# Kernel optimization log

Hardware: AMD Instinct MI355X
Metric: run time of the kernel (lower is better)

Reference implementation:

```python
import jax, jax.numpy as jnp
import numpy as np


def _degree_norms(src, dst, num_nodes, dtype):
    ones = jnp.ones(src.shape[0], dtype=dtype)
    out_deg = jax.ops.segment_sum(ones, src, num_segments=num_nodes)
    in_deg = jax.ops.segment_sum(ones, dst, num_segments=num_nodes)
    # DGL clamps degrees to min 1 (allow_zero_in_degree=True path)
    norm_src = jax.lax.rsqrt(jnp.maximum(out_deg, 1.0))  # D_out^{-1/2}
    norm_dst = jax.lax.rsqrt(jnp.maximum(in_deg, 1.0))   # D_in^{-1/2}
    return norm_src, norm_dst


def _graph_conv(x, W, b, src, dst, norm_src, norm_dst, num_nodes):
    # h = D_in^{-1/2} A D_out^{-1/2} x W + b  (DGL GraphConv, norm='both')
    h = x * norm_src[:, None]                                   # [N, d_in]
    agg = jax.ops.segment_sum(h[src], dst, num_segments=num_nodes)  # gather-scatter SpMM
    agg = agg * norm_dst[:, None]
    return agg @ W + b


def setup_inputs() -> dict:
    key = jax.random.key(0)
    k1, k2, k3, k4, k5 = jax.random.split(key, 5)
    N, E, D_IN, D_OUT = 100000, 1600000, 128, 64
    feature = jax.random.normal(k1, (N, D_IN), dtype=jnp.float32)
    src = jax.random.randint(k2, (E,), 0, N, dtype=jnp.int64)
    dst = jax.random.randint(k3, (E,), 0, N, dtype=jnp.int64)
    W1 = jax.random.normal(k4, (D_IN, D_IN), dtype=jnp.float32) / np.sqrt(D_IN)
    b1 = jnp.zeros((D_IN,), dtype=jnp.float32)
    W2 = jax.random.normal(k5, (D_IN, D_OUT), dtype=jnp.float32) / np.sqrt(D_IN)
    b2 = jnp.zeros((D_OUT,), dtype=jnp.float32)
    return {"feature": feature, "src": src, "dst": dst,
            "W1": W1, "b1": b1, "W2": W2, "b2": b2}


def reference(feature, src, dst, W1, b1, W2, b2):
    N = feature.shape[0]
    norm_src, norm_dst = _degree_norms(src, dst, N, feature.dtype)
    out = _graph_conv(feature, W1, b1, src, dst, norm_src, norm_dst, N)
    out = jax.nn.relu(out)
    # dropout is identity in eval mode (correctness baseline)
    out = _graph_conv(out, W2, b2, src, dst, norm_src, norm_dst, N)
    return out
```

## Files before the change

kernel.cpp:

```cpp
#include <hip/hip_runtime.h>

#define DIN 128
#define PB 512
typedef unsigned short u16;
typedef unsigned int u32;
typedef __attribute__((ext_vector_type(8))) short bf16x8;
typedef __attribute__((ext_vector_type(4))) float f32x4;

static __device__ __forceinline__ float bf2f(u32 lo16) {
    union { u32 u; float f; } c;
    c.u = lo16 << 16;
    return c.f;
}
static __device__ __forceinline__ float bf_lo(u32 v) {
    union { u32 u; float f; } c;
    c.u = v << 16;
    return c.f;
}
static __device__ __forceinline__ float bf_hi(u32 v) {
    union { u32 u; float f; } c;
    c.u = v & 0xffff0000u;
    return c.f;
}
static __device__ __forceinline__ u32 f2bf(float f) {
    union { float f; u32 u; } c;
    c.f = f;
    u32 u = c.u;
    u += 0x7fffu + ((u >> 16) & 1u);
    return u >> 16;
}

static __device__ __forceinline__ int wave_incl_scan(int x, int lane) {
#pragma unroll
    for (int off = 1; off < 64; off <<= 1) {
        int y = __shfl_up(x, off, 64);
        if (lane >= off) x += y;
    }
    return x;
}

__global__ __launch_bounds__(256) void hist_kernel(
    const int* __restrict__ src, const int* __restrict__ dst,
    u32* __restrict__ mat, int E, int NB, int M) {
    __shared__ u32 hd[512], hs[512];
    int t = threadIdx.x, b = blockIdx.x;
    for (int j = t; j < NB; j += 256) { hd[j] = 0; hs[j] = 0; }
    __syncthreads();
    int chunk = (E + PB - 1) / PB;
    int s = b * chunk, e = min(E, s + chunk);
    for (int i = s + t; i < e; i += 256) {
        atomicAdd(&hd[((u32)dst[i]) >> 8], 1u);
        atomicAdd(&hs[((u32)src[i]) >> 8], 1u);
    }
    __syncthreads();
    for (int j = t; j < NB; j += 256) {
        mat[(size_t)j * PB + b] = hd[j];
        mat[(size_t)M + (size_t)j * PB + b] = hs[j];
    }
}

__global__ void scan_block_kernel(const int* __restrict__ in, int* __restrict__ out,
                                  int* __restrict__ bsums, int n) {
    __shared__ int wsum[4];
    int i = blockIdx.x * 256 + threadIdx.x;
    int lane = threadIdx.x & 63, wid = threadIdx.x >> 6;
    int v = (i < n) ? in[i] : 0;
    int sc = wave_incl_scan(v, lane);
    if (lane == 63) wsum[wid] = sc;
    __syncthreads();
    int add = 0;
    for (int w = 0; w < wid; ++w) add += wsum[w];
    if (i < n) out[i] = sc - v + add;
    if (threadIdx.x == 255) bsums[blockIdx.x] = sc + add;
}

__global__ void scan_sums_kernel(int* __restrict__ bsums, int nb) {
    __shared__ int wsum[4];
    __shared__ int carry;
    int lane = threadIdx.x & 63, wid = threadIdx.x >> 6;
    if (threadIdx.x == 0) carry = 0;
    __syncthreads();
    for (int base = 0; base < nb; base += 256) {
        int i = base + threadIdx.x;
        int v = (i < nb) ? bsums[i] : 0;
        int sc = wave_incl_scan(v, lane);
        if (lane == 63) wsum[wid] = sc;
        __syncthreads();
        int add = carry;
        for (int w = 0; w < wid; ++w) add += wsum[w];
        if (i < nb) bsums[i] = sc - v + add;
        __syncthreads();
        if (threadIdx.x == 0) carry += wsum[0] + wsum[1] + wsum[2] + wsum[3];
        __syncthreads();
    }
}

__global__ void add_off2_kernel(int* __restrict__ out, const int* __restrict__ bsums, int n) {
    int i = blockIdx.x * 256 + threadIdx.x;
    if (i < n) out[i] += bsums[i >> 8];
}

__global__ __launch_bounds__(256) void part_kernel(
    const int* __restrict__ src, const int* __restrict__ dst,
    const int* __restrict__ off, u32* __restrict__ part, int E, int NB, int M) {
    __shared__ u32 cd[512], cs[512];
    int t = threadIdx.x, b = blockIdx.x;
    for (int j = t; j < NB; j += 256) {
        cd[j] = (u32)off[(size_t)j * PB + b];
        cs[j] = (u32)off[(size_t)M + (size_t)j * PB + b];
    }
    __syncthreads();
    int chunk = (E + PB - 1) / PB;
    int s = b * chunk, e = min(E, s + chunk);
    for (int i = s + t; i < e; i += 256) {
        u32 dv = (u32)dst[i], sv = (u32)src[i];
        u32 p = atomicAdd(&cd[dv >> 8], 1u);
        part[p] = ((dv & 255u) << 24) | sv;
        u32 q = atomicAdd(&cs[sv >> 8], 1u);
        part[q] = sv;
    }
}

__global__ __launch_bounds__(256) void build_kernel(
    const u32* __restrict__ part, const int* __restrict__ off,
    int* __restrict__ rowptr, float* __restrict__ nd, float* __restrict__ ns,
    int* __restrict__ csr_src, int N, int E, int NB, int M) {
    __shared__ u32 lh[256];
    __shared__ u32 cur[256];
    __shared__ int wsum[4];
    int t = threadIdx.x, k = blockIdx.x;
    int lane = t & 63, wid = t >> 6;
    int node = k * 256 + t;

    int beg = off[(size_t)k * PB];
    int end = (k + 1 < NB) ? off[(size_t)(k + 1) * PB] : E;

    lh[t] = 0;
    __syncthreads();
    for (int i = beg + t; i < end; i += 256)
        atomicAdd(&lh[part[i] >> 24], 1u);
    __syncthreads();

    int cnt = (int)lh[t];
    int sc = wave_incl_scan(cnt, lane);
    if (lane == 63) wsum[wid] = sc;
    __syncthreads();
    int add = 0;
    for (int w = 0; w < wid; ++w) add += wsum[w];
    int ex = sc - cnt + add;

    if (node < N) {
        rowptr[node] = beg + ex;
        nd[node] = rsqrtf(fmaxf((float)cnt, 1.0f));
    }
    if (k == 0 && t == 0) rowptr[N] = E;
    cur[t] = (u32)(beg + ex);
    __syncthreads();

    for (int i = beg + t; i < end; i += 256) {
        u32 v = part[i];
        u32 pos = atomicAdd(&cur[v >> 24], 1u);
        csr_src[pos] = (int)(v & 0xFFFFFFu);
    }

    int beg2 = off[(size_t)M + (size_t)k * PB];
    int end2 = (k + 1 < NB) ? off[(size_t)M + (size_t)(k + 1) * PB] : 2 * E;
    __syncthreads();
    lh[t] = 0;
    __syncthreads();
    for (int i = beg2 + t; i < end2; i += 256)
        atomicAdd(&lh[part[i] & 255u], 1u);
    __syncthreads();
    if (node < N) ns[node] = rsqrtf(fmaxf((float)lh[t], 1.0f));
}

__global__ __launch_bounds__(256, 8) void gather128_kernel(
    const uint2* __restrict__ tp, const int* __restrict__ rowptr,
    const int* __restrict__ csr_src, const float* __restrict__ nd,
    const float* __restrict__ bias, uint2* __restrict__ out, int N) {
    int tid = threadIdx.x;
    int lane = tid & 63;
    int half = lane >> 5;
    int w = lane & 31;
    int node = blockIdx.x * 8 + ((tid >> 6) << 1) + half;
    bool valid = node < N;
    int nc = valid ? node : 0;
    int beg = rowptr[nc];
    int cnt = valid ? (rowptr[nc + 1] - beg) : 0;
    const int* ip = csr_src + beg;

    float a0 = 0.f, a1 = 0.f, a2 = 0.f, a3 = 0.f;
    int j = 0;
    for (; j + 8 <= cnt; j += 8) {
        int s[8];
#pragma unroll
        for (int k = 0; k < 8; ++k) s[k] = ip[j + k];
        uint2 v[8];
#pragma unroll
        for (int k = 0; k < 8; ++k) v[k] = tp[(size_t)s[k] * 32 + w];
#pragma unroll
        for (int k = 0; k < 8; ++k) {
            a0 += bf_lo(v[k].x); a1 += bf_hi(v[k].x);
            a2 += bf_lo(v[k].y); a3 += bf_hi(v[k].y);
        }
    }
    if (j + 4 <= cnt) {
        int s[4];
#pragma unroll
        for (int k = 0; k < 4; ++k) s[k] = ip[j + k];
        uint2 v[4];
#pragma unroll
        for (int k = 0; k < 4; ++k) v[k] = tp[(size_t)s[k] * 32 + w];
#pragma unroll
        for (int k = 0; k < 4; ++k) {
            a0 += bf_lo(v[k].x); a1 += bf_hi(v[k].x);
            a2 += bf_lo(v[k].y); a3 += bf_hi(v[k].y);
        }
        j += 4;
    }
    if (j + 2 <= cnt) {
        uint2 v0 = tp[(size_t)ip[j] * 32 + w];
        uint2 v1 = tp[(size_t)ip[j + 1] * 32 + w];
        a0 += bf_lo(v0.x) + bf_lo(v1.x); a1 += bf_hi(v0.x) + bf_hi(v1.x);
        a2 += bf_lo(v0.y) + bf_lo(v1.y); a3 += bf_hi(v0.y) + bf_hi(v1.y);
        j += 2;
    }
    if (j < cnt) {
        uint2 v0 = tp[(size_t)ip[j] * 32 + w];
        a0 += bf_lo(v0.x); a1 += bf_hi(v0.x);
        a2 += bf_lo(v0.y); a3 += bf_hi(v0.y);
    }

    if (valid) {
        float sc = nd[nc];
        float4 bv = reinterpret_cast<const float4*>(bias)[w];
        float r0 = fmaxf(a0 * sc + bv.x, 0.f);
        float r1 = fmaxf(a1 * sc + bv.y, 0.f);
        float r2 = fmaxf(a2 * sc + bv.z, 0.f);
        float r3 = fmaxf(a3 * sc + bv.w, 0.f);
        uint2 o;
        o.x = f2bf(r0) | (f2bf(r1) << 16);
        o.y = f2bf(r2) | (f2bf(r3) << 16);
        out[(size_t)node * 32 + w] = o;
    }
}

__global__ __launch_bounds__(256, 8) void gather64_kernel(
    const u32* __restrict__ tp, const int* __restrict__ rowptr,
    const int* __restrict__ csr_src, const float* __restrict__ nd,
    const float* __restrict__ bias, float2* __restrict__ out, int N) {
    int tid = threadIdx.x;
    int lane = tid & 63;
    int half = lane >> 5;
    int w = lane & 31;
    int node = blockIdx.x * 8 + ((tid >> 6) << 1) + half;
    bool valid = node < N;
    int nc = valid ? node : 0;
    int beg = rowptr[nc];
    int cnt = valid ? (rowptr[nc + 1] - beg) : 0;
    const int* ip = csr_src + beg;

    float a0 = 0.f, a1 = 0.f;
    int j = 0;
    for (; j + 8 <= cnt; j += 8) {
        int s[8];
#pragma unroll
        for (int k = 0; k < 8; ++k) s[k] = ip[j + k];
        u32 v[8];
#pragma unroll
        for (int k = 0; k < 8; ++k) v[k] = tp[(size_t)s[k] * 32 + w];
#pragma unroll
        for (int k = 0; k < 8; ++k) { a0 += bf_lo(v[k]); a1 += bf_hi(v[k]); }
    }
    if (j + 4 <= cnt) {
        int s[4];
#pragma unroll
        for (int k = 0; k < 4; ++k) s[k] = ip[j + k];
        u32 v[4];
#pragma unroll
        for (int k = 0; k < 4; ++k) v[k] = tp[(size_t)s[k] * 32 + w];
#pragma unroll
        for (int k = 0; k < 4; ++k) { a0 += bf_lo(v[k]); a1 += bf_hi(v[k]); }
        j += 4;
    }
    if (j + 2 <= cnt) {
        u32 v0 = tp[(size_t)ip[j] * 32 + w];
        u32 v1 = tp[(size_t)ip[j + 1] * 32 + w];
        a0 += bf_lo(v0) + bf_lo(v1);
        a1 += bf_hi(v0) + bf_hi(v1);
        j += 2;
    }
    if (j < cnt) {
        u32 v0 = tp[(size_t)ip[j] * 32 + w];
        a0 += bf_lo(v0); a1 += bf_hi(v0);
    }

    if (valid) {
        float sc = nd[nc];
        float2 bv = reinterpret_cast<const float2*>(bias)[w];
        float2 o;
        o.x = a0 * sc + bv.x;
        o.y = a1 * sc + bv.y;
        out[(size_t)node * 32 + w] = o;
    }
}

template <int DOUT, bool ABF16>
__global__ __launch_bounds__(256) void gemm_mfma_kernel(
    const void* __restrict__ Av, const float* __restrict__ W,
    const float* __restrict__ scale, u16* __restrict__ out, int n) {
    constexpr int NT = DOUT / 16;
    constexpr int WK = DIN + 8;
    __shared__ u16 Wt[DOUT * WK];

    for (int i = threadIdx.x; i < DIN * DOUT; i += 256) {
        int k = i / DOUT, c = i % DOUT;
        Wt[c * WK + k] = (u16)f2bf(W[i]);
    }

    int lane = threadIdx.x & 63;
    int wid = threadIdx.x >> 6;
    int row = blockIdx.x * 64 + wid * 16 + (lane & 15);
    int rc = min(row, n - 1);
    int kg = lane >> 4;

    bf16x8 afrag[4];
    if (ABF16) {
        const u16* ap = (const u16*)Av + (size_t)rc * DIN + kg * 8;
#pragma unroll
        for (int s = 0; s < 4; ++s) {
            uint4 v = *reinterpret_cast<const uint4*>(ap + s * 32);
            afrag[s] = *reinterpret_cast<bf16x8*>(&v);
        }
    } else {
        const float* ap = (const float*)Av + (size_t)rc * DIN + kg * 8;
#pragma unroll
        for (int s = 0; s < 4; ++s) {
            float4 v0 = *reinterpret_cast<const float4*>(ap + s * 32);
            float4 v1 = *reinterpret_cast<const float4*>(ap + s * 32 + 4);
            uint4 v;
            v.x = f2bf(v0.x) | (f2bf(v0.y) << 16);
            v.y = f2bf(v0.z) | (f2bf(v0.w) << 16);
            v.z = f2bf(v1.x) | (f2bf(v1.y) << 16);
            v.w = f2bf(v1.z) | (f2bf(v1.w) << 16);
            afrag[s] = *reinterpret_cast<bf16x8*>(&v);
        }
    }

    f32x4 acc[NT];
#pragma unroll
    for (int t = 0; t < NT; ++t) acc[t] = (f32x4){0.f, 0.f, 0.f, 0.f};

    __syncthreads();

#pragma unroll
    for (int t = 0; t < NT; ++t) {
        const u16* wp = Wt + (t * 16 + (lane & 15)) * WK + kg * 8;
#pragma unroll
        for (int s = 0; s < 4; ++s) {
            uint4 wv = *reinterpret_cast<const uint4*>(wp + s * 32);
            bf16x8 wfrag = *reinterpret_cast<bf16x8*>(&wv);
            acc[t] = __builtin_amdgcn_mfma_f32_16x16x32_bf16(wfrag, afrag[s], acc[t], 0, 0, 0);
        }
    }

    if (row < n) {
        float sc = scale[row];
        u16* op = out + (size_t)row * DOUT + kg * 4;
#pragma unroll
        for (int t = 0; t < NT; ++t) {
            uint2 v;
            v.x = f2bf(acc[t][0] * sc) | (f2bf(acc[t][1] * sc) << 16);
            v.y = f2bf(acc[t][2] * sc) | (f2bf(acc[t][3] * sc) << 16);
            *reinterpret_cast<uint2*>(op + t * 16) = v;
        }
    }
}

extern "C" void kernel_launch(void* const* d_in, const int* in_sizes, int n_in,
                              void* d_out, int out_size, void* d_ws, size_t ws_size,
                              hipStream_t stream) {
    const float* feature = (const float*)d_in[0];
    const int*   src     = (const int*)d_in[1];
    const int*   dst     = (const int*)d_in[2];
    const float* W1      = (const float*)d_in[3];
    const float* b1      = (const float*)d_in[4];
    const float* W2      = (const float*)d_in[5];
    const float* b2      = (const float*)d_in[6];

    const int N = in_sizes[0] / DIN;
    const int E = in_sizes[1];
    const int NB = (N + 255) >> 8;
    const int M = NB * PB;
    const int M2 = 2 * M;
    const int nbm = (M2 + 255) / 256;

    char* ws = (char*)d_ws;
    size_t off_b = 0;
    auto take = [&](size_t bytes) -> void* {
        void* p = ws + off_b;
        off_b += (bytes + 255) & ~(size_t)255;
        return p;
    };
    float* ns      = (float*)take((size_t)N * 4);
    float* nd      = (float*)take((size_t)N * 4);
    int*   rowptr  = (int*)take((size_t)(N + 1) * 4);
    int*   csr_src = (int*)take((size_t)E * 4);
    u32*   mat     = (u32*)take((size_t)M2 * 4);
    int*   off     = (int*)take((size_t)M2 * 4);
    int*   bs      = (int*)take((size_t)(nbm + 4) * 4);
    u32*   part    = (u32*)take((size_t)2 * E * 4);
    u16*   t1      = (u16*)take((size_t)N * DIN * 2);
    u16*   h2      = (u16*)take((size_t)N * DIN * 2);

    hist_kernel<<<PB, 256, 0, stream>>>(src, dst, mat, E, NB, M);
    scan_block_kernel<<<nbm, 256, 0, stream>>>((const int*)mat, off, bs, M2);
    scan_sums_kernel<<<1, 256, 0, stream>>>(bs, nbm);
    add_off2_kernel<<<nbm, 256, 0, stream>>>(off, bs, M2);
    part_kernel<<<PB, 256, 0, stream>>>(src, dst, off, part, E, NB, M);
    build_kernel<<<NB, 256, 0, stream>>>(part, off, rowptr, nd, ns, csr_src, N, E, NB, M);

    gemm_mfma_kernel<128, false><<<(N + 63) / 64, 256, 0, stream>>>(feature, W1, ns, t1, N);
    gather128_kernel<<<(N + 7) / 8, 256, 0, stream>>>(
        (const uint2*)t1, rowptr, csr_src, nd, b1, (uint2*)h2, N);

    gemm_mfma_kernel<64, true><<<(N + 63) / 64, 256, 0, stream>>>(h2, W2, ns, t1, N);
    gather64_kernel<<<(N + 7) / 8, 256, 0, stream>>>(
        (const u32*)t1, rowptr, csr_src, nd, b2, (float2*)d_out, N);
}
```

Baseline: 209.4 us.

## Slice feature tables column-wise so each gather block touches a cache-sized slice

The GEMM outputs and the layer-1 hidden features are now stored as 8 column slices (16 or 8 bf16 per node per slice). Each gather block handles one slice for many nodes, so the random-access working set per slice is N*32 bytes (or N*16) and can stay in L2/MALL. The cost is 8x more index and rowptr reads, narrower per-lane 4-byte loads with 8 or 4 lanes per row (short coalesced segments), and less unrolling in the gather loops.

```diff
diff --git a/kernel.cpp b/kernel.cpp
--- a/kernel.cpp
+++ b/kernel.cpp
@@ -7,11 +7,6 @@
 typedef __attribute__((ext_vector_type(8))) short bf16x8;
 typedef __attribute__((ext_vector_type(4))) float f32x4;
 
-static __device__ __forceinline__ float bf2f(u32 lo16) {
-    union { u32 u; float f; } c;
-    c.u = lo16 << 16;
-    return c.f;
-}
 static __device__ __forceinline__ float bf_lo(u32 v) {
     union { u32 u; float f; } c;
     c.u = v << 16;
@@ -174,141 +169,98 @@
     if (node < N) ns[node] = rsqrtf(fmaxf((float)lh[t], 1.0f));
 }
 
-__global__ __launch_bounds__(256, 8) void gather128_kernel(
-    const uint2* __restrict__ tp, const int* __restrict__ rowptr,
+__global__ __launch_bounds__(256, 8) void gather128s_kernel(
+    const u32* __restrict__ tsl, const int* __restrict__ rowptr,
     const int* __restrict__ csr_src, const float* __restrict__ nd,
-    const float* __restrict__ bias, uint2* __restrict__ out, int N) {
+    const float* __restrict__ bias, u32* __restrict__ h2sl, int N) {
+    int bid = blockIdx.x;
+    int slice = bid & 7;
+    int nb = bid >> 3;
     int tid = threadIdx.x;
-    int lane = tid & 63;
-    int half = lane >> 5;
-    int w = lane & 31;
-    int node = blockIdx.x * 8 + ((tid >> 6) << 1) + half;
+    int g = tid >> 3;
+    int w = tid & 7;
+    int node = nb * 32 + g;
     bool valid = node < N;
     int nc = valid ? node : 0;
     int beg = rowptr[nc];
     int cnt = valid ? (rowptr[nc + 1] - beg) : 0;
     const int* ip = csr_src + beg;
-
-    float a0 = 0.f, a1 = 0.f, a2 = 0.f, a3 = 0.f;
+    const u32* ts = tsl + (size_t)slice * N * 8;
+
+    float a0 = 0.f, a1 = 0.f;
     int j = 0;
-    for (; j + 8 <= cnt; j += 8) {
-        int s[8];
-#pragma unroll
-        for (int k = 0; k < 8; ++k) s[k] = ip[j + k];
-        uint2 v[8];
-#pragma unroll
-        for (int k = 0; k < 8; ++k) v[k] = tp[(size_t)s[k] * 32 + w];
-#pragma unroll
-        for (int k = 0; k < 8; ++k) {
-            a0 += bf_lo(v[k].x); a1 += bf_hi(v[k].x);
-            a2 += bf_lo(v[k].y); a3 += bf_hi(v[k].y);
-        }
-    }
-    if (j + 4 <= cnt) {
-        int s[4];
-#pragma unroll
-        for (int k = 0; k < 4; ++k) s[k] = ip[j + k];
-        uint2 v[4];
-#pragma unroll
-        for (int k = 0; k < 4; ++k) v[k] = tp[(size_t)s[k] * 32 + w];
-#pragma unroll
-        for (int k = 0; k < 4; ++k) {
-            a0 += bf_lo(v[k].x); a1 += bf_hi(v[k].x);
-            a2 += bf_lo(v[k].y); a3 += bf_hi(v[k].y);
-        }
-        j += 4;
-    }
-    if (j + 2 <= cnt) {
-        uint2 v0 = tp[(size_t)ip[j] * 32 + w];
-        uint2 v1 = tp[(size_t)ip[j + 1] * 32 + w];
-        a0 += bf_lo(v0.x) + bf_lo(v1.x); a1 += bf_hi(v0.x) + bf_hi(v1.x);
-        a2 += bf_lo(v0.y) + bf_lo(v1.y); a3 += bf_hi(v0.y) + bf_hi(v1.y);
-        j += 2;
-    }
-    if (j < cnt) {
-        uint2 v0 = tp[(size_t)ip[j] * 32 + w];
-        a0 += bf_lo(v0.x); a1 += bf_hi(v0.x);
-        a2 += bf_lo(v0.y); a3 += bf_hi(v0.y);
+    for (; j + 4 <= cnt; j += 4) {
+        int s0 = ip[j], s1 = ip[j + 1], s2 = ip[j + 2], s3 = ip[j + 3];
+        u32 v0 = ts[s0 * 8 + w];
+        u32 v1 = ts[s1 * 8 + w];
+        u32 v2 = ts[s2 * 8 + w];
+        u32 v3 = ts[s3 * 8 + w];
+        a0 += bf_lo(v0) + bf_lo(v1) + bf_lo(v2) + bf_lo(v3);
+        a1 += bf_hi(v0) + bf_hi(v1) + bf_hi(v2) + bf_hi(v3);
+    }
+    for (; j < cnt; ++j) {
+        u32 v = ts[ip[j] * 8 + w];
+        a0 += bf_lo(v); a1 += bf_hi(v);
     }
 
     if (valid) {
         float sc = nd[nc];
-        float4 bv = reinterpret_cast<const float4*>(bias)[w];
-        float r0 = fmaxf(a0 * sc + bv.x, 0.f);
-        float r1 = fmaxf(a1 * sc + bv.y, 0.f);
-        float r2 = fmaxf(a2 * sc + bv.z, 0.f);
-        float r3 = fmaxf(a3 * sc + bv.w, 0.f);
-        uint2 o;
-        o.x = f2bf(r0) | (f2bf(r1) << 16);
-        o.y = f2bf(r2) | (f2bf(r3) << 16);
-        out[(size_t)node * 32 + w] = o;
-    }
-}
-
-__global__ __launch_bounds__(256, 8) void gather64_kernel(
-    const u32* __restrict__ tp, const int* __restrict__ rowptr,
+        float2 bv = reinterpret_cast<const float2*>(bias)[slice * 8 + w];
+        float r0 = fmaxf(fmaf(a0, sc, bv.x), 0.f);
+        float r1 = fmaxf(fmaf(a1, sc, bv.y), 0.f);
+        h2sl[(size_t)slice * N * 8 + (size_t)node * 8 + w] = f2bf(r0) | (f2bf(r1) << 16);
+    }
+}
+
+__global__ __launch_bounds__(256, 8) void gather64s_kernel(
+    const u32* __restrict__ tsl, const int* __restrict__ rowptr,
     const int* __restrict__ csr_src, const float* __restrict__ nd,
-    const float* __restrict__ bias, float2* __restrict__ out, int N) {
+    const float* __restrict__ bias, float* __restrict__ out, int N) {
+    int bid = blockIdx.x;
+    int slice = bid & 7;
+    int nb = bid >> 3;
     int tid = threadIdx.x;
-    int lane = tid & 63;
-    int half = lane >> 5;
-    int w = lane & 31;
-    int node = blockIdx.x * 8 + ((tid >> 6) << 1) + half;
+    int g = tid >> 2;
+    int w = tid & 3;
+    int node = nb * 64 + g;
     bool valid = node < N;
     int nc = valid ? node : 0;
     int beg = rowptr[nc];
     int cnt = valid ? (rowptr[nc + 1] - beg) : 0;
     const int* ip = csr_src + beg;
+    const u32* ts = tsl + (size_t)slice * N * 4;
 
     float a0 = 0.f, a1 = 0.f;
     int j = 0;
-    for (; j + 8 <= cnt; j += 8) {
-        int s[8];
-#pragma unroll
-        for (int k = 0; k < 8; ++k) s[k] = ip[j + k];
-        u32 v[8];
-#pragma unroll
-        for (int k = 0; k < 8; ++k) v[k] = tp[(size_t)s[k] * 32 + w];
-#pragma unroll
-        for (int k = 0; k < 8; ++k) { a0 += bf_lo(v[k]); a1 += bf_hi(v[k]); }
-    }
-    if (j + 4 <= cnt) {
-        int s[4];
-#pragma unroll
-        for (int k = 0; k < 4; ++k) s[k] = ip[j + k];
-        u32 v[4];
-#pragma unroll
-        for (int k = 0; k < 4; ++k) v[k] = tp[(size_t)s[k] * 32 + w];
-#pragma unroll
-        for (int k = 0; k < 4; ++k) { a0 += bf_lo(v[k]); a1 += bf_hi(v[k]); }
-        j += 4;
-    }
-    if (j + 2 <= cnt) {
-        u32 v0 = tp[(size_t)ip[j] * 32 + w];
-        u32 v1 = tp[(size_t)ip[j + 1] * 32 + w];
-        a0 += bf_lo(v0) + bf_lo(v1);
-        a1 += bf_hi(v0) + bf_hi(v1);
-        j += 2;
-    }
-    if (j < cnt) {
-        u32 v0 = tp[(size_t)ip[j] * 32 + w];
-        a0 += bf_lo(v0); a1 += bf_hi(v0);
+    for (; j + 4 <= cnt; j += 4) {
+        int s0 = ip[j], s1 = ip[j + 1], s2 = ip[j + 2], s3 = ip[j + 3];
+        u32 v0 = ts[s0 * 4 + w];
+        u32 v1 = ts[s1 * 4 + w];
+        u32 v2 = ts[s2 * 4 + w];
+        u32 v3 = ts[s3 * 4 + w];
+        a0 += bf_lo(v0) + bf_lo(v1) + bf_lo(v2) + bf_lo(v3);
+        a1 += bf_hi(v0) + bf_hi(v1) + bf_hi(v2) + bf_hi(v3);
+    }
+    for (; j < cnt; ++j) {
+        u32 v = ts[ip[j] * 4 + w];
+        a0 += bf_lo(v); a1 += bf_hi(v);
     }
 
     if (valid) {
         float sc = nd[nc];
-        float2 bv = reinterpret_cast<const float2*>(bias)[w];
+        float2 bv = reinterpret_cast<const float2*>(bias)[slice * 4 + w];
         float2 o;
-        o.x = a0 * sc + bv.x;
-        o.y = a1 * sc + bv.y;
-        out[(size_t)node * 32 + w] = o;
-    }
-}
-
-template <int DOUT, bool ABF16>
+        o.x = fmaf(a0, sc, bv.x);
+        o.y = fmaf(a1, sc, bv.y);
+        *reinterpret_cast<float2*>(out + (size_t)node * 64 + slice * 8 + 2 * w) = o;
+    }
+}
+
+template <bool LAYER2>
 __global__ __launch_bounds__(256) void gemm_mfma_kernel(
     const void* __restrict__ Av, const float* __restrict__ W,
     const float* __restrict__ scale, u16* __restrict__ out, int n) {
+    constexpr int DOUT = LAYER2 ? 64 : 128;
     constexpr int NT = DOUT / 16;
     constexpr int WK = DIN + 8;
     __shared__ u16 Wt[DOUT * WK];
@@ -325,11 +277,12 @@
     int kg = lane >> 4;
 
     bf16x8 afrag[4];
-    if (ABF16) {
-        const u16* ap = (const u16*)Av + (size_t)rc * DIN + kg * 8;
+    if (LAYER2) {
+        const u16* ap = (const u16*)Av;
 #pragma unroll
         for (int s = 0; s < 4; ++s) {
-            uint4 v = *reinterpret_cast<const uint4*>(ap + s * 32);
+            const u16* p = ap + (size_t)(2 * s + (kg >> 1)) * n * 16 + (size_t)rc * 16 + (kg & 1) * 8;
+            uint4 v = *reinterpret_cast<const uint4*>(p);
             afrag[s] = *reinterpret_cast<bf16x8*>(&v);
         }
     } else {
@@ -366,13 +319,17 @@
 
     if (row < n) {
         float sc = scale[row];
-        u16* op = out + (size_t)row * DOUT + kg * 4;
+        uint2* ob = reinterpret_cast<uint2*>(out);
 #pragma unroll
         for (int t = 0; t < NT; ++t) {
             uint2 v;
             v.x = f2bf(acc[t][0] * sc) | (f2bf(acc[t][1] * sc) << 16);
             v.y = f2bf(acc[t][2] * sc) | (f2bf(acc[t][3] * sc) << 16);
-            *reinterpret_cast<uint2*>(op + t * 16) = v;
+            if (LAYER2) {
+                ob[(size_t)(2 * t + (kg >> 1)) * n * 2 + (size_t)row * 2 + (kg & 1)] = v;
+            } else {
+                ob[(size_t)t * n * 4 + (size_t)row * 4 + kg] = v;
+            }
         }
     }
 }
@@ -420,11 +377,11 @@
     part_kernel<<<PB, 256, 0, stream>>>(src, dst, off, part, E, NB, M);
     build_kernel<<<NB, 256, 0, stream>>>(part, off, rowptr, nd, ns, csr_src, N, E, NB, M);
 
-    gemm_mfma_kernel<128, false><<<(N + 63) / 64, 256, 0, stream>>>(feature, W1, ns, t1, N);
-    gather128_kernel<<<(N + 7) / 8, 256, 0, stream>>>(
-        (const uint2*)t1, rowptr, csr_src, nd, b1, (uint2*)h2, N);
-
-    gemm_mfma_kernel<64, true><<<(N + 63) / 64, 256, 0, stream>>>(h2, W2, ns, t1, N);
-    gather64_kernel<<<(N + 7) / 8, 256, 0, stream>>>(
-        (const u32*)t1, rowptr, csr_src, nd, b2, (float2*)d_out, N);
-}
+    gemm_mfma_kernel<false><<<(N + 63) / 64, 256, 0, stream>>>(feature, W1, ns, t1, N);
+    gather128s_kernel<<<8 * ((N + 31) / 32), 256, 0, stream>>>(
+        (const u32*)t1, rowptr, csr_src, nd, b1, (u32*)h2, N);
+
+    gemm_mfma_kernel<true><<<(N + 63) / 64, 256, 0, stream>>>(h2, W2, ns, t1, N);
+    gather64s_kernel<<<8 * ((N + 63) / 64), 256, 0, stream>>>(
+        (const u32*)t1, rowptr, csr_src, nd, b2, (float*)d_out, N);
+}
```

Measured after the change: 268.2 us. 1.28x slower.

## Slice layer-1 features into column slabs for cache-resident gathers

Applied to the files above, without the earlier changes.

The first GEMM now writes its bf16 output as eight column slices of 16 features each, and the layer-1 gather launches one block per (node group, slice), so each gather pass touches only one 3.2MB slab that can stay in L2. The second GEMM reads the sliced layout back. The layer-2 gather switches to 16 lanes per node with 8-byte loads and float4 stores. The cost is eight times more reads of the CSR index lists and only 32-byte reads per neighbor per slice, which may lower memory efficiency.

```diff
diff --git a/kernel.cpp b/kernel.cpp
--- a/kernel.cpp
+++ b/kernel.cpp
@@ -7,11 +7,6 @@
 typedef __attribute__((ext_vector_type(8))) short bf16x8;
 typedef __attribute__((ext_vector_type(4))) float f32x4;
 
-static __device__ __forceinline__ float bf2f(u32 lo16) {
-    union { u32 u; float f; } c;
-    c.u = lo16 << 16;
-    return c.f;
-}
 static __device__ __forceinline__ float bf_lo(u32 v) {
     union { u32 u; float f; } c;
     c.u = v << 16;
@@ -174,141 +169,138 @@
     if (node < N) ns[node] = rsqrtf(fmaxf((float)lh[t], 1.0f));
 }
 
-__global__ __launch_bounds__(256, 8) void gather128_kernel(
-    const uint2* __restrict__ tp, const int* __restrict__ rowptr,
+__global__ __launch_bounds__(256, 8) void gather128s_kernel(
+    const u32* __restrict__ tsl, const int* __restrict__ rowptr,
     const int* __restrict__ csr_src, const float* __restrict__ nd,
-    const float* __restrict__ bias, uint2* __restrict__ out, int N) {
+    const float* __restrict__ bias, u32* __restrict__ h2sl, int N) {
+    int bid = blockIdx.x;
+    int slice = bid & 7;
+    int nb = bid >> 3;
     int tid = threadIdx.x;
-    int lane = tid & 63;
-    int half = lane >> 5;
-    int w = lane & 31;
-    int node = blockIdx.x * 8 + ((tid >> 6) << 1) + half;
+    int g = tid >> 3;
+    int w = tid & 7;
+    int node = nb * 32 + g;
     bool valid = node < N;
     int nc = valid ? node : 0;
     int beg = rowptr[nc];
     int cnt = valid ? (rowptr[nc + 1] - beg) : 0;
     const int* ip = csr_src + beg;
-
-    float a0 = 0.f, a1 = 0.f, a2 = 0.f, a3 = 0.f;
+    const u32* ts = tsl + (size_t)slice * N * 8 + w;
+
+    float a0 = 0.f, a1 = 0.f;
     int j = 0;
     for (; j + 8 <= cnt; j += 8) {
-        int s[8];
+        int s[8]; u32 v[8];
 #pragma unroll
         for (int k = 0; k < 8; ++k) s[k] = ip[j + k];
-        uint2 v[8];
-#pragma unroll
-        for (int k = 0; k < 8; ++k) v[k] = tp[(size_t)s[k] * 32 + w];
-#pragma unroll
-        for (int k = 0; k < 8; ++k) {
-            a0 += bf_lo(v[k].x); a1 += bf_hi(v[k].x);
-            a2 += bf_lo(v[k].y); a3 += bf_hi(v[k].y);
-        }
+#pragma unroll
+        for (int k = 0; k < 8; ++k) v[k] = ts[(size_t)s[k] * 8];
+#pragma unroll
+        for (int k = 0; k < 8; ++k) { a0 += bf_lo(v[k]); a1 += bf_hi(v[k]); }
     }
     if (j + 4 <= cnt) {
-        int s[4];
+        int s[4]; u32 v[4];
 #pragma unroll
         for (int k = 0; k < 4; ++k) s[k] = ip[j + k];
-        uint2 v[4];
-#pragma unroll
-        for (int k = 0; k < 4; ++k) v[k] = tp[(size_t)s[k] * 32 + w];
-#pragma unroll
-        for (int k = 0; k < 4; ++k) {
-            a0 += bf_lo(v[k].x); a1 += bf_hi(v[k].x);
-            a2 += bf_lo(v[k].y); a3 += bf_hi(v[k].y);
-        }
+#pragma unroll
+        for (int k = 0; k < 4; ++k) v[k] = ts[(size_t)s[k] * 8];
+#pragma unroll
+        for (int k = 0; k < 4; ++k) { a0 += bf_lo(v[k]); a1 += bf_hi(v[k]); }
         j += 4;
     }
     if (j + 2 <= cnt) {
-        uint2 v0 = tp[(size_t)ip[j] * 32 + w];
-        uint2 v1 = tp[(size_t)ip[j + 1] * 32 + w];
-        a0 += bf_lo(v0.x) + bf_lo(v1.x); a1 += bf_hi(v0.x) + bf_hi(v1.x);
-        a2 += bf_lo(v0.y) + bf_lo(v1.y); a3 += bf_hi(v0.y) + bf_hi(v1.y);
+        u32 v0 = ts[(size_t)ip[j] * 8];
+        u32 v1 = ts[(size_t)ip[j + 1] * 8];
+        a0 += bf_lo(v0) + bf_lo(v1);
+        a1 += bf_hi(v0) + bf_hi(v1);
         j += 2;
     }
     if (j < cnt) {
-        uint2 v0 = tp[(size_t)ip[j] * 32 + w];
-        a0 += bf_lo(v0.x); a1 += bf_hi(v0.x);
-        a2 += bf_lo(v0.y); a3 += bf_hi(v0.y);
+        u32 v0 = ts[(size_t)ip[j] * 8];
+        a0 += bf_lo(v0); a1 += bf_hi(v0);
     }
 
     if (valid) {
         float sc = nd[nc];
-        float4 bv = reinterpret_cast<const float4*>(bias)[w];
-        float r0 = fmaxf(a0 * sc + bv.x, 0.f);
-        float r1 = fmaxf(a1 * sc + bv.y, 0.f);
-        float r2 = fmaxf(a2 * sc + bv.z, 0.f);
-        float r3 = fmaxf(a3 * sc + bv.w, 0.f);
-        uint2 o;
-        o.x = f2bf(r0) | (f2bf(r1) << 16);
-        o.y = f2bf(r2) | (f2bf(r3) << 16);
-        out[(size_t)node * 32 + w] = o;
+        float2 bv = reinterpret_cast<const float2*>(bias)[slice * 8 + w];
+        float r0 = fmaxf(fmaf(a0, sc, bv.x), 0.f);
+        float r1 = fmaxf(fmaf(a1, sc, bv.y), 0.f);
+        h2sl[(size_t)slice * N * 8 + (size_t)node * 8 + w] = f2bf(r0) | (f2bf(r1) << 16);
     }
 }
 
 __global__ __launch_bounds__(256, 8) void gather64_kernel(
-    const u32* __restrict__ tp, const int* __restrict__ rowptr,
+    const uint2* __restrict__ tp, const int* __restrict__ rowptr,
     const int* __restrict__ csr_src, const float* __restrict__ nd,
-    const float* __restrict__ bias, float2* __restrict__ out, int N) {
+    const float* __restrict__ bias, float* __restrict__ out, int N) {
     int tid = threadIdx.x;
-    int lane = tid & 63;
-    int half = lane >> 5;
-    int w = lane & 31;
-    int node = blockIdx.x * 8 + ((tid >> 6) << 1) + half;
+    int g = tid >> 4;
+    int w = tid & 15;
+    int node = blockIdx.x * 16 + g;
     bool valid = node < N;
     int nc = valid ? node : 0;
     int beg = rowptr[nc];
     int cnt = valid ? (rowptr[nc + 1] - beg) : 0;
     const int* ip = csr_src + beg;
-
-    float a0 = 0.f, a1 = 0.f;
+    const uint2* ts = tp + w;
+
+    float a0 = 0.f, a1 = 0.f, a2 = 0.f, a3 = 0.f;
     int j = 0;
     for (; j + 8 <= cnt; j += 8) {
-        int s[8];
+        int s[8]; uint2 v[8];
 #pragma unroll
         for (int k = 0; k < 8; ++k) s[k] = ip[j + k];
-        u32 v[8];
-#pragma unroll
-        for (int k = 0; k < 8; ++k) v[k] = tp[(size_t)s[k] * 32 + w];
-#pragma unroll
-        for (int k = 0; k < 8; ++k) { a0 += bf_lo(v[k]); a1 += bf_hi(v[k]); }
+#pragma unroll
+        for (int k = 0; k < 8; ++k) v[k] = ts[(size_t)s[k] * 16];
+#pragma unroll
+        for (int k = 0; k < 8; ++k) {
+            a0 += bf_lo(v[k].x); a1 += bf_hi(v[k].x);
+            a2 += bf_lo(v[k].y); a3 += bf_hi(v[k].y);
+        }
     }
     if (j + 4 <= cnt) {
-        int s[4];
+        int s[4]; uint2 v[4];
 #pragma unroll
         for (int k = 0; k < 4; ++k) s[k] = ip[j + k];
-        u32 v[4];
-#pragma unroll
-        for (int k = 0; k < 4; ++k) v[k] = tp[(size_t)s[k] * 32 + w];
-#pragma unroll
-        for (int k = 0; k < 4; ++k) { a0 += bf_lo(v[k]); a1 += bf_hi(v[k]); }
+#pragma unroll
+        for (int k = 0; k < 4; ++k) v[k] = ts[(size_t)s[k] * 16];
+#pragma unroll
+        for (int k = 0; k < 4; ++k) {
+            a0 += bf_lo(v[k].x); a1 += bf_hi(v[k].x);
+            a2 += bf_lo(v[k].y); a3 += bf_hi(v[k].y);
+        }
         j += 4;
     }
     if (j + 2 <= cnt) {
-        u32 v0 = tp[(size_t)ip[j] * 32 + w];
-        u32 v1 = tp[(size_t)ip[j + 1] * 32 + w];
-        a0 += bf_lo(v0) + bf_lo(v1);
-        a1 += bf_hi(v0) + bf_hi(v1);
+        uint2 v0 = ts[(size_t)ip[j] * 16];
+        uint2 v1 = ts[(size_t)ip[j + 1] * 16];
+        a0 += bf_lo(v0.x) + bf_lo(v1.x); a1 += bf_hi(v0.x) + bf_hi(v1.x);
+        a2 += bf_lo(v0.y) + bf_lo(v1.y); a3 += bf_hi(v0.y) + bf_hi(v1.y);
         j += 2;
     }
     if (j < cnt) {
-        u32 v0 = tp[(size_t)ip[j] * 32 + w];
-        a0 += bf_lo(v0); a1 += bf_hi(v0);
+        uint2 v0 = ts[(size_t)ip[j] * 16];
+        a0 += bf_lo(v0.x); a1 += bf_hi(v0.x);
+        a2 += bf_lo(v0.y); a3 += bf_hi(v0.y);
     }
 
     if (valid) {
         float sc = nd[nc];
-        float2 bv = reinterpret_cast<const float2*>(bias)[w];
-        float2 o;
-        o.x = a0 * sc + bv.x;
-        o.y = a1 * sc + bv.y;
-        out[(size_t)node * 32 + w] = o;
-    }
-}
-
-template <int DOUT, bool ABF16>
+        float4 bv = reinterpret_cast<const float4*>(bias)[w];
+        float4 o;
+        o.x = fmaf(a0, sc, bv.x);
+        o.y = fmaf(a1, sc, bv.y);
+        o.z = fmaf(a2, sc, bv.z);
+        o.w = fmaf(a3, sc, bv.w);
+        *reinterpret_cast<float4*>(out + (size_t)node * 64 + 4 * w) = o;
+    }
+}
+
+template <bool LAYER2>
 __global__ __launch_bounds__(256) void gemm_mfma_kernel(
     const void* __restrict__ Av, const float* __restrict__ W,
     const float* __restrict__ scale, u16* __restrict__ out, int n) {
+    constexpr int DOUT = LAYER2 ? 64 : 128;
     constexpr int NT = DOUT / 16;
     constexpr int WK = DIN + 8;
     __shared__ u16 Wt[DOUT * WK];
@@ -325,11 +317,12 @@
     int kg = lane >> 4;
 
     bf16x8 afrag[4];
-    if (ABF16) {
-        const u16* ap = (const u16*)Av + (size_t)rc * DIN + kg * 8;
+    if (LAYER2) {
+        const u16* ap = (const u16*)Av;
 #pragma unroll
         for (int s = 0; s < 4; ++s) {
-            uint4 v = *reinterpret_cast<const uint4*>(ap + s * 32);
+            const u16* p = ap + (size_t)(2 * s + (kg >> 1)) * n * 16 + (size_t)rc * 16 + (kg & 1) * 8;
+            uint4 v = *reinterpret_cast<const uint4*>(p);
             afrag[s] = *reinterpret_cast<bf16x8*>(&v);
         }
     } else {
@@ -366,13 +359,16 @@
 
     if (row < n) {
         float sc = scale[row];
-        u16* op = out + (size_t)row * DOUT + kg * 4;
 #pragma unroll
         for (int t = 0; t < NT; ++t) {
             uint2 v;
             v.x = f2bf(acc[t][0] * sc) | (f2bf(acc[t][1] * sc) << 16);
             v.y = f2bf(acc[t][2] * sc) | (f2bf(acc[t][3] * sc) << 16);
-            *reinterpret_cast<uint2*>(op + t * 16) = v;
+            if (LAYER2) {
+                *reinterpret_cast<uint2*>(out + (size_t)row * 64 + t * 16 + kg * 4) = v;
+            } else {
+                reinterpret_cast<uint2*>(out)[(size_t)t * n * 4 + (size_t)row * 4 + kg] = v;
+            }
         }
     }
 }
@@ -420,11 +416,11 @@
     part_kernel<<<PB, 256, 0, stream>>>(src, dst, off, part, E, NB, M);
     build_kernel<<<NB, 256, 0, stream>>>(part, off, rowptr, nd, ns, csr_src, N, E, NB, M);
 
-    gemm_mfma_kernel<128, false><<<(N + 63) / 64, 256, 0, stream>>>(feature, W1, ns, t1, N);
-    gather128_kernel<<<(N + 7) / 8, 256, 0, stream>>>(
-        (const uint2*)t1, rowptr, csr_src, nd, b1, (uint2*)h2, N);
-
-    gemm_mfma_kernel<64, true><<<(N + 63) / 64, 256, 0, stream>>>(h2, W2, ns, t1, N);
-    gather64_kernel<<<(N + 7) / 8, 256, 0, stream>>>(
-        (const u32*)t1, rowptr, csr_src, nd, b2, (float2*)d_out, N);
-}
+    gemm_mfma_kernel<false><<<(N + 63) / 64, 256, 0, stream>>>(feature, W1, ns, t1, N);
+    gather128s_kernel<<<8 * ((N + 31) / 32), 256, 0, stream>>>(
+        (const u32*)t1, rowptr, csr_src, nd, b1, (u32*)h2, N);
+
+    gemm_mfma_kernel<true><<<(N + 63) / 64, 256, 0, stream>>>(h2, W2, ns, t1, N);
+    gather64_kernel<<<(N + 15) / 16, 256, 0, stream>>>(
+        (const uint2*)t1, rowptr, csr_src, nd, b2, (float*)d_out, N);
+}
```

Result: slower. 222.9 us (+6.4%).
